# Kernel optimization log

Hardware: AMD Instinct MI355X
Metric: run time of the kernel (lower is better)

## Reference

```python
import jax, jax.numpy as jnp
import numpy as np

EPS = 1e-8


def kabsch_align(P, Q):
    """Align P to Q per the original torch code. P, Q: [B, N, 3].

    Note: the torch code unpacks torch.linalg.svd as (U, S, V) where the third
    return is actually Vh; we faithfully reproduce that exact math.
    """
    P_mean = jnp.mean(P, axis=1, keepdims=True)          # [B,1,3]
    Q_mean = jnp.mean(Q, axis=1, keepdims=True)
    P_c = P - P_mean
    Q_c = Q - Q_mean
    H = jnp.einsum('bni,bnj->bij', P_c, Q_c)             # [B,3,3] covariance
    U, S, Vh = jnp.linalg.svd(H, full_matrices=False)
    Ut = jnp.swapaxes(U, 1, 2)
    d = jnp.linalg.det(jnp.matmul(Vh, Ut))               # [B]
    e = jnp.stack([jnp.ones_like(d), jnp.ones_like(d), d], axis=-1)  # diag(1,1,d)
    R = jnp.einsum('bik,bk,bkj->bij', Vh, e, Ut)         # [B,3,3]
    # P_aligned = P_c @ R^T + Q_mean
    return jnp.einsum('bni,bji->bnj', P_c, R) + Q_mean


def setup_inputs() -> dict:
    key = jax.random.key(0)
    k1, k2 = jax.random.split(key)
    B, K, N = 256, 5, 4096
    preds = jax.random.normal(k1, (B, K, N, 3), dtype=jnp.float32)
    target = jax.random.normal(k2, (B, N, 3), dtype=jnp.float32)
    return {"preds": preds, "target": target}


def reference(preds, target):
    B, K, N, _ = preds.shape
    P = preds.reshape(B * K, N, 3)
    Q = jnp.broadcast_to(target[:, None], (B, K, N, 3)).reshape(B * K, N, 3)
    aligned = kabsch_align(P, Q)                         # [B*K, N, 3]
    mse = jnp.mean((aligned - Q) ** 2, axis=(1, 2))      # [B*K]
    rmsd = jnp.sqrt(mse + EPS).reshape(B, K)
    return jnp.mean(jnp.min(rmsd, axis=1))
```

## Files before the change

### kernel.cpp

```cpp
#include <hip/hip_runtime.h>
#include <math.h>

#define B_    256
#define K_    5
#define N_    4096
#define NPAIR (B_ * K_)
#define NMOM  17

__device__ inline void cross3f(const float* a, const float* b, float* c) {
  c[0] = a[1] * b[2] - a[2] * b[1];
  c[1] = a[2] * b[0] - a[0] * b[2];
  c[2] = a[0] * b[1] - a[1] * b[0];
}
__device__ inline float dot3f(const float* a, const float* b) {
  return a[0] * b[0] + a[1] * b[1] + a[2] * b[2];
}
__device__ inline void fixsign3f(float* v) {
  const float a0 = fabsf(v[0]), a1 = fabsf(v[1]), a2 = fabsf(v[2]);
  const int i = (a0 >= a1 && a0 >= a2) ? 0 : ((a1 >= a2) ? 1 : 2);
  if (v[i] < 0.f) { v[0] = -v[0]; v[1] = -v[1]; v[2] = -v[2]; }
}
__device__ inline void eigvec3f(const float A[3][3], float lam, float* v) {
  const float r0[3] = {A[0][0] - lam, A[0][1], A[0][2]};
  const float r1[3] = {A[1][0], A[1][1] - lam, A[1][2]};
  const float r2[3] = {A[2][0], A[2][1], A[2][2] - lam};
  float c01[3], c02[3], c12[3];
  cross3f(r0, r1, c01); cross3f(r0, r2, c02); cross3f(r1, r2, c12);
  const float n01 = dot3f(c01, c01), n02 = dot3f(c02, c02), n12 = dot3f(c12, c12);
  const float* best = c01; float nb = n01;
  if (n02 > nb) { best = c02; nb = n02; }
  if (n12 > nb) { best = c12; nb = n12; }
  if (nb < 1e-30f) { v[0] = 1.f; v[1] = 0.f; v[2] = 0.f; return; }
  const float inv = 1.f / sqrtf(nb);
  v[0] = best[0] * inv; v[1] = best[1] * inv; v[2] = best[2] * inv;
}

__device__ inline float svd_rmsd(const float* m) {
  const float invN = 1.f / (float)N_;
  const float sP[3] = {m[0], m[1], m[2]};
  const float sQ[3] = {m[3], m[4], m[5]};
  float H[3][3];
#pragma unroll
  for (int i = 0; i < 3; ++i)
#pragma unroll
    for (int j = 0; j < 3; ++j)
      H[i][j] = m[8 + 3 * i + j] - sP[i] * sQ[j] * invN;

  const float Sp = m[6] - dot3f(sP, sP) * invN;
  const float Sq = m[7] - dot3f(sQ, sQ) * invN;

  float A[3][3];
#pragma unroll
  for (int i = 0; i < 3; ++i)
#pragma unroll
    for (int j = 0; j < 3; ++j)
      A[i][j] = H[0][i] * H[0][j] + H[1][i] * H[1][j] + H[2][i] * H[2][j];

  float lam[3];
  float V[3][3];
  const float q = (A[0][0] + A[1][1] + A[2][2]) * (1.f / 3.f);
  const float p1 = A[0][1] * A[0][1] + A[0][2] * A[0][2] + A[1][2] * A[1][2];
  const float p2 = (A[0][0] - q) * (A[0][0] - q) +
                   (A[1][1] - q) * (A[1][1] - q) +
                   (A[2][2] - q) * (A[2][2] - q) + 2.f * p1;
  if (p2 < 1e-20f) {
    lam[0] = lam[1] = lam[2] = q;
#pragma unroll
    for (int i = 0; i < 3; ++i)
#pragma unroll
      for (int j = 0; j < 3; ++j) V[i][j] = (i == j) ? 1.f : 0.f;
  } else {
    const float p = sqrtf(p2 * (1.f / 6.f));
    const float invp = 1.f / p;
    float Bm[3][3];
#pragma unroll
    for (int i = 0; i < 3; ++i)
#pragma unroll
      for (int j = 0; j < 3; ++j)
        Bm[i][j] = (A[i][j] - ((i == j) ? q : 0.f)) * invp;
    const float detB =
        Bm[0][0] * (Bm[1][1] * Bm[2][2] - Bm[1][2] * Bm[2][1]) -
        Bm[0][1] * (Bm[1][0] * Bm[2][2] - Bm[1][2] * Bm[2][0]) +
        Bm[0][2] * (Bm[1][0] * Bm[2][1] - Bm[1][1] * Bm[2][0]);
    float r = detB * 0.5f;
    r = fminf(1.f, fmaxf(-1.f, r));
    const float phi = acosf(r) * (1.f / 3.f);
    lam[0] = q + 2.f * p * cosf(phi);
    lam[2] = q + 2.f * p * cosf(phi + 2.0943951023931953f);
    lam[1] = 3.f * q - lam[0] - lam[2];

    float v1[3], v2[3], v3[3];
    eigvec3f(A, lam[0], v1);
    eigvec3f(A, lam[1], v2);
    const float d12 = dot3f(v1, v2);
    v2[0] -= d12 * v1[0]; v2[1] -= d12 * v1[1]; v2[2] -= d12 * v1[2];
    float n2 = dot3f(v2, v2);
    if (n2 < 1e-12f) {
      const float a0 = fabsf(v1[0]), a1f = fabsf(v1[1]), a2f = fabsf(v1[2]);
      int ax = (a0 <= a1f && a0 <= a2f) ? 0 : ((a1f <= a2f) ? 1 : 2);
      float e[3] = {0.f, 0.f, 0.f};
      e[ax] = 1.f;
      const float de = dot3f(v1, e);
      v2[0] = e[0] - de * v1[0]; v2[1] = e[1] - de * v1[1]; v2[2] = e[2] - de * v1[2];
      n2 = dot3f(v2, v2);
    }
    const float invn2 = 1.f / sqrtf(n2);
    v2[0] *= invn2; v2[1] *= invn2; v2[2] *= invn2;

    fixsign3f(v1);
    fixsign3f(v2);
    cross3f(v1, v2, v3);
#pragma unroll
    for (int i = 0; i < 3; ++i) { V[i][0] = v1[i]; V[i][1] = v2[i]; V[i][2] = v3[i]; }
  }

  const float S0 = sqrtf(fmaxf(lam[0], 0.f));
  const float S1 = sqrtf(fmaxf(lam[1], 0.f));
  const float S2 = sqrtf(fmaxf(lam[2], 0.f));

  const float detH =
      H[0][0] * (H[1][1] * H[2][2] - H[1][2] * H[2][1]) -
      H[0][1] * (H[1][0] * H[2][2] - H[1][2] * H[2][0]) +
      H[0][2] * (H[1][0] * H[2][1] - H[1][1] * H[2][0]);
  const float dsg = (detH >= 0.f) ? 1.f : -1.f;

  const float M00 = V[0][0] * V[0][0] + V[1][0] * V[0][1] + V[2][0] * V[0][2];
  const float M11 = V[0][1] * V[1][0] + V[1][1] * V[1][1] + V[2][1] * V[1][2];
  const float M22 = V[0][2] * V[2][0] + V[1][2] * V[2][1] + V[2][2] * V[2][2];

  const float T = S0 * M00 + S1 * M11 + dsg * S2 * M22;
  const float mse = (Sp + Sq - 2.f * T) * (1.f / (3.f * (float)N_));
  return sqrtf(mse + 1e-8f);
}

__global__ __launch_bounds__(256) void kabsch_moments_svd(
    const float* __restrict__ preds, const float* __restrict__ target,
    float* __restrict__ rmsd) {
  const int idx = blockIdx.x;
  const int b = idx & 255;
  const int k = idx >> 8;
  const int pair_orig = b * K_ + k;
  const int tid = threadIdx.x;

  const float4* __restrict__ P4 =
      reinterpret_cast<const float4*>(preds) + (size_t)pair_orig * (N_ * 3 / 4);
  const float4* __restrict__ Q4 =
      reinterpret_cast<const float4*>(target) + (size_t)b * (N_ * 3 / 4);

  float acc[NMOM];
#pragma unroll
  for (int i = 0; i < NMOM; ++i) acc[i] = 0.f;

#pragma unroll
  for (int j = 0; j < 4; ++j) {
    const int c = tid + j * 256;
    const float4 a0 = P4[3 * c + 0], a1 = P4[3 * c + 1], a2 = P4[3 * c + 2];
    const float4 b0 = Q4[3 * c + 0], b1 = Q4[3 * c + 1], b2 = Q4[3 * c + 2];
    const float p[4][3] = {{a0.x, a0.y, a0.z},
                           {a0.w, a1.x, a1.y},
                           {a1.z, a1.w, a2.x},
                           {a2.y, a2.z, a2.w}};
    const float q[4][3] = {{b0.x, b0.y, b0.z},
                           {b0.w, b1.x, b1.y},
                           {b1.z, b1.w, b2.x},
                           {b2.y, b2.z, b2.w}};
#pragma unroll
    for (int m = 0; m < 4; ++m) {
      const float px = p[m][0], py = p[m][1], pz = p[m][2];
      const float qx = q[m][0], qy = q[m][1], qz = q[m][2];
      acc[0] += px; acc[1] += py; acc[2] += pz;
      acc[3] += qx; acc[4] += qy; acc[5] += qz;
      acc[6] = fmaf(px, px, fmaf(py, py, fmaf(pz, pz, acc[6])));
      acc[7] = fmaf(qx, qx, fmaf(qy, qy, fmaf(qz, qz, acc[7])));
      acc[8]  = fmaf(px, qx, acc[8]);
      acc[9]  = fmaf(px, qy, acc[9]);
      acc[10] = fmaf(px, qz, acc[10]);
      acc[11] = fmaf(py, qx, acc[11]);
      acc[12] = fmaf(py, qy, acc[12]);
      acc[13] = fmaf(py, qz, acc[13]);
      acc[14] = fmaf(pz, qx, acc[14]);
      acc[15] = fmaf(pz, qy, acc[15]);
      acc[16] = fmaf(pz, qz, acc[16]);
    }
  }

#pragma unroll
  for (int off = 32; off > 0; off >>= 1) {
#pragma unroll
    for (int i = 0; i < NMOM; ++i) acc[i] += __shfl_down(acc[i], off, 64);
  }

  __shared__ float red[4][NMOM];
  const int lane = tid & 63, wid = tid >> 6;
  if (lane == 0) {
#pragma unroll
    for (int i = 0; i < NMOM; ++i) red[wid][i] = acc[i];
  }
  __syncthreads();

  if (tid == 0) {
    float m[NMOM];
#pragma unroll
    for (int i = 0; i < NMOM; ++i)
      m[i] = red[0][i] + red[1][i] + red[2][i] + red[3][i];
    rmsd[idx] = svd_rmsd(m);
  }
}

__global__ __launch_bounds__(256) void kabsch_final(
    const float* __restrict__ rmsd, float* __restrict__ out) {
  const int b = threadIdx.x;
  float mn = rmsd[b];
#pragma unroll
  for (int k = 1; k < K_; ++k) mn = fminf(mn, rmsd[k * 256 + b]);
#pragma unroll
  for (int off = 32; off > 0; off >>= 1) mn += __shfl_down(mn, off, 64);
  __shared__ float s[4];
  if ((b & 63) == 0) s[b >> 6] = mn;
  __syncthreads();
  if (b == 0) out[0] = (s[0] + s[1] + s[2] + s[3]) * (1.0f / 256.0f);
}

extern "C" void kernel_launch(void* const* d_in, const int* in_sizes, int n_in,
                              void* d_out, int out_size, void* d_ws, size_t ws_size,
                              hipStream_t stream) {
  const float* preds = (const float*)d_in[0];
  const float* target = (const float*)d_in[1];
  float* out = (float*)d_out;
  float* rm = (float*)d_ws;

  hipLaunchKernelGGL(kabsch_moments_svd, dim3(NPAIR), dim3(256), 0, stream,
                     preds, target, rm);
  hipLaunchKernelGGL(kabsch_final, dim3(1), dim3(256), 0, stream, rm, out);
}
```

Before: 22.09 us.

## Process all K predictions per block to reuse target loads

Restructures the moment kernel so one 512-thread block per batch element loads the target once and accumulates moments for all five predictions, instead of one block per (b,k) pair. This removes the redundant target reads. In exchange it raises the per-thread accumulator count to 69, lengthens the shuffle reduction, and cuts the grid to 256 blocks, which lowers occupancy and may limit memory-level parallelism.

```diff
diff --git a/kernel.cpp b/kernel.cpp
--- a/kernel.cpp
+++ b/kernel.cpp
@@ -5,7 +5,7 @@
 #define K_    5
 #define N_    4096
 #define NPAIR (B_ * K_)
-#define NMOM  17
+#define NACC  69
 
 __device__ inline void cross3f(const float* a, const float* b, float* c) {
   c[0] = a[1] * b[2] - a[2] * b[1];
@@ -133,77 +133,102 @@
   return sqrtf(mse + 1e-8f);
 }
 
-__global__ __launch_bounds__(256) void kabsch_moments_svd(
+__global__ __launch_bounds__(512) void kabsch_moments_svd(
     const float* __restrict__ preds, const float* __restrict__ target,
     float* __restrict__ rmsd) {
-  const int idx = blockIdx.x;
-  const int b = idx & 255;
-  const int k = idx >> 8;
-  const int pair_orig = b * K_ + k;
+  const int b = blockIdx.x;
   const int tid = threadIdx.x;
 
-  const float4* __restrict__ P4 =
-      reinterpret_cast<const float4*>(preds) + (size_t)pair_orig * (N_ * 3 / 4);
   const float4* __restrict__ Q4 =
       reinterpret_cast<const float4*>(target) + (size_t)b * (N_ * 3 / 4);
-
-  float acc[NMOM];
-#pragma unroll
-  for (int i = 0; i < NMOM; ++i) acc[i] = 0.f;
-
-#pragma unroll
-  for (int j = 0; j < 4; ++j) {
-    const int c = tid + j * 256;
-    const float4 a0 = P4[3 * c + 0], a1 = P4[3 * c + 1], a2 = P4[3 * c + 2];
-    const float4 b0 = Q4[3 * c + 0], b1 = Q4[3 * c + 1], b2 = Q4[3 * c + 2];
-    const float p[4][3] = {{a0.x, a0.y, a0.z},
-                           {a0.w, a1.x, a1.y},
-                           {a1.z, a1.w, a2.x},
-                           {a2.y, a2.z, a2.w}};
-    const float q[4][3] = {{b0.x, b0.y, b0.z},
-                           {b0.w, b1.x, b1.y},
-                           {b1.z, b1.w, b2.x},
-                           {b2.y, b2.z, b2.w}};
+  const float4* __restrict__ P4 =
+      reinterpret_cast<const float4*>(preds) +
+      (size_t)b * K_ * (N_ * 3 / 4);
+
+  float acc[NACC];
+#pragma unroll
+  for (int i = 0; i < NACC; ++i) acc[i] = 0.f;
+
+#pragma unroll
+  for (int it = 0; it < 2; ++it) {
+    const int c = tid + it * 512;
+
+    const float4 q0 = Q4[3 * c + 0], q1 = Q4[3 * c + 1], q2 = Q4[3 * c + 2];
+    float4 pA[5], pB[5], pC[5];
+#pragma unroll
+    for (int k = 0; k < K_; ++k) {
+      const float4* Pk = P4 + (size_t)k * (N_ * 3 / 4);
+      pA[k] = Pk[3 * c + 0]; pB[k] = Pk[3 * c + 1]; pC[k] = Pk[3 * c + 2];
+    }
+
+    const float qq[4][3] = {{q0.x, q0.y, q0.z},
+                            {q0.w, q1.x, q1.y},
+                            {q1.z, q1.w, q2.x},
+                            {q2.y, q2.z, q2.w}};
 #pragma unroll
     for (int m = 0; m < 4; ++m) {
-      const float px = p[m][0], py = p[m][1], pz = p[m][2];
-      const float qx = q[m][0], qy = q[m][1], qz = q[m][2];
-      acc[0] += px; acc[1] += py; acc[2] += pz;
-      acc[3] += qx; acc[4] += qy; acc[5] += qz;
-      acc[6] = fmaf(px, px, fmaf(py, py, fmaf(pz, pz, acc[6])));
-      acc[7] = fmaf(qx, qx, fmaf(qy, qy, fmaf(qz, qz, acc[7])));
-      acc[8]  = fmaf(px, qx, acc[8]);
-      acc[9]  = fmaf(px, qy, acc[9]);
-      acc[10] = fmaf(px, qz, acc[10]);
-      acc[11] = fmaf(py, qx, acc[11]);
-      acc[12] = fmaf(py, qy, acc[12]);
-      acc[13] = fmaf(py, qz, acc[13]);
-      acc[14] = fmaf(pz, qx, acc[14]);
-      acc[15] = fmaf(pz, qy, acc[15]);
-      acc[16] = fmaf(pz, qz, acc[16]);
+      const float qx = qq[m][0], qy = qq[m][1], qz = qq[m][2];
+      acc[0] += qx; acc[1] += qy; acc[2] += qz;
+      acc[3] = fmaf(qx, qx, fmaf(qy, qy, fmaf(qz, qz, acc[3])));
+    }
+#pragma unroll
+    for (int k = 0; k < K_; ++k) {
+      const float pp[4][3] = {{pA[k].x, pA[k].y, pA[k].z},
+                              {pA[k].w, pB[k].x, pB[k].y},
+                              {pB[k].z, pB[k].w, pC[k].x},
+                              {pC[k].y, pC[k].z, pC[k].w}};
+      const int o = 4 + 13 * k;
+#pragma unroll
+      for (int m = 0; m < 4; ++m) {
+        const float px = pp[m][0], py = pp[m][1], pz = pp[m][2];
+        const float qx = qq[m][0], qy = qq[m][1], qz = qq[m][2];
+        acc[o + 0] += px; acc[o + 1] += py; acc[o + 2] += pz;
+        acc[o + 3] = fmaf(px, px, fmaf(py, py, fmaf(pz, pz, acc[o + 3])));
+        acc[o + 4]  = fmaf(px, qx, acc[o + 4]);
+        acc[o + 5]  = fmaf(px, qy, acc[o + 5]);
+        acc[o + 6]  = fmaf(px, qz, acc[o + 6]);
+        acc[o + 7]  = fmaf(py, qx, acc[o + 7]);
+        acc[o + 8]  = fmaf(py, qy, acc[o + 8]);
+        acc[o + 9]  = fmaf(py, qz, acc[o + 9]);
+        acc[o + 10] = fmaf(pz, qx, acc[o + 10]);
+        acc[o + 11] = fmaf(pz, qy, acc[o + 11]);
+        acc[o + 12] = fmaf(pz, qz, acc[o + 12]);
+      }
     }
   }
 
 #pragma unroll
   for (int off = 32; off > 0; off >>= 1) {
 #pragma unroll
-    for (int i = 0; i < NMOM; ++i) acc[i] += __shfl_down(acc[i], off, 64);
-  }
-
-  __shared__ float red[4][NMOM];
+    for (int i = 0; i < NACC; ++i) acc[i] += __shfl_down(acc[i], off, 64);
+  }
+
+  __shared__ float red[8][NACC];
+  __shared__ float fin[NACC];
   const int lane = tid & 63, wid = tid >> 6;
   if (lane == 0) {
 #pragma unroll
-    for (int i = 0; i < NMOM; ++i) red[wid][i] = acc[i];
+    for (int i = 0; i < NACC; ++i) red[wid][i] = acc[i];
   }
   __syncthreads();
-
-  if (tid == 0) {
-    float m[NMOM];
-#pragma unroll
-    for (int i = 0; i < NMOM; ++i)
-      m[i] = red[0][i] + red[1][i] + red[2][i] + red[3][i];
-    rmsd[idx] = svd_rmsd(m);
+  if (tid < NACC) {
+    float s = 0.f;
+#pragma unroll
+    for (int w = 0; w < 8; ++w) s += red[w][tid];
+    fin[tid] = s;
+  }
+  __syncthreads();
+
+  if (tid < K_) {
+    const int o = 4 + 13 * tid;
+    float m[17];
+    m[0] = fin[o + 0]; m[1] = fin[o + 1]; m[2] = fin[o + 2];
+    m[3] = fin[0];     m[4] = fin[1];     m[5] = fin[2];
+    m[6] = fin[o + 3];
+    m[7] = fin[3];
+#pragma unroll
+    for (int i = 0; i < 9; ++i) m[8 + i] = fin[o + 4 + i];
+    rmsd[tid * 256 + b] = svd_rmsd(m);
   }
 }
 
@@ -229,7 +254,7 @@
   float* out = (float*)d_out;
   float* rm = (float*)d_ws;
 
-  hipLaunchKernelGGL(kabsch_moments_svd, dim3(NPAIR), dim3(256), 0, stream,
+  hipLaunchKernelGGL(kabsch_moments_svd, dim3(B_), dim3(512), 0, stream,
                      preds, target, rm);
   hipLaunchKernelGGL(kabsch_final, dim3(1), dim3(256), 0, stream, rm, out);
 }
```

Result: slower. 29.30 us, median of 2 (+32.7%).
